# Performance work log

Measured on AMD Instinct MI355X. Metric: run time of the kernel, lower is better.

Reference implementation:

```python
import jax, jax.numpy as jnp
import numpy as np

G = 8          # grid_size
N = G * G      # 64 nodes
DEG = 17       # neighbors per node for 8x8 sudoku (2x4 boxes)
STEPS = 32
H = 96         # hidden_dim
E = 16         # embed_size
B = 16         # batch


def sudoku_edges():
    # row (7) + col (7) + 2x4 box (7) neighbors, set-union -> 17 per node
    idx = np.arange(N).reshape(G, G)
    nb = []
    for j in range(N):
        r, c = j // G, j % G
        br, bc = (r // 2) * 2, (c // 4) * 4
        s = set(idx[r, :].tolist()) | set(idx[:, c].tolist()) | set(idx[br:br + 2, bc:bc + 4].flatten().tolist())
        s.discard(j)
        nb.append(sorted(s))
    return np.asarray(nb, dtype=np.int32)  # [64, 17]


def setup_inputs() -> dict:
    key = jax.random.key(0)
    ks = jax.random.split(key, 16)
    sc = 0.05
    inp = {
        "x": jax.random.randint(ks[0], (B, G, G), 0, G + 1),            # given digits, 0 = blank
        "target": jax.random.randint(ks[1], (B, G, G), 0, G) + 1,       # solutions in 1..8
        "edges": jnp.asarray(sudoku_edges()),                            # [64, 17] int32
        "digit_emb": jax.random.normal(ks[2], (G + 1, E), jnp.float32) * sc,
        "row_emb": jax.random.normal(ks[3], (G, E), jnp.float32) * sc,
        "col_emb": jax.random.normal(ks[4], (G, E), jnp.float32) * sc,
        "in0_W": jax.random.normal(ks[5], (3 * E, H), jnp.float32) * sc,
        "in0_b": jnp.zeros((H,), jnp.float32),
        "in_Ws": jax.random.normal(ks[6], (3, H, H), jnp.float32) * sc,
        "in_bs": jnp.zeros((3, H), jnp.float32),
        "msg0_W": jax.random.normal(ks[7], (2 * H, H), jnp.float32) * sc,
        "msg0_b": jnp.zeros((H,), jnp.float32),
        "msg_Ws": jax.random.normal(ks[8], (3, H, H), jnp.float32) * sc,
        "msg_bs": jnp.zeros((3, H), jnp.float32),
        "W_ih": jax.random.normal(ks[9], (2 * H, 4 * H), jnp.float32) * sc,
        "W_hh": jax.random.normal(ks[10], (H, 4 * H), jnp.float32) * sc,
        "b_ih": jnp.zeros((4 * H,), jnp.float32),
        "b_hh": jnp.zeros((4 * H,), jnp.float32),
        "pred_W": jax.random.normal(ks[11], (H, G), jnp.float32) * sc,
        "pred_b": jnp.zeros((G,), jnp.float32),
    }
    return inp


def _mlp(z, W0, b0, Ws, bs):
    # Linear -> ReLU -> Linear -> ReLU -> Linear -> ReLU -> Linear (def_MLP)
    z = jax.nn.relu(z @ W0 + b0)
    z = jax.nn.relu(z @ Ws[0] + bs[0])
    z = jax.nn.relu(z @ Ws[1] + bs[1])
    return z @ Ws[2] + bs[2]


def reference(x, target, edges, digit_emb, row_emb, col_emb,
              in0_W, in0_b, in_Ws, in_bs,
              msg0_W, msg0_b, msg_Ws, msg_bs,
              W_ih, W_hh, b_ih, b_hh, pred_W, pred_b):
    bsz = x.shape[0]
    xf = x.reshape(bsz, N)
    tgt = target.reshape(bsz, N) - 1                      # labels 0..7

    de = digit_emb[xf]                                    # [B,64,E]
    re = row_emb[jnp.repeat(jnp.arange(G), G)]            # [64,E]
    ce = col_emb[jnp.tile(jnp.arange(G), G)]              # [64,E]
    feat = jnp.concatenate([de,
                            jnp.broadcast_to(re[None], (bsz, N, E)),
                            jnp.broadcast_to(ce[None], (bsz, N, E))], axis=-1)
    xin = _mlp(feat, in0_W, in0_b, in_Ws, in_bs)          # [B,64,H]

    h0 = jnp.zeros((bsz, N, H), jnp.float32)
    s0 = jnp.zeros((bsz * N, H), jnp.float32)

    def step(carry, _):
        h, s, loss = carry
        # gather-by-edge message passing
        h_edges = h[:, edges]                                             # [B,64,17,H]
        h_self = jnp.broadcast_to(h[:, :, None, :], (bsz, N, DEG, H))
        msg = _mlp(jnp.concatenate([h_edges, h_self], -1),
                   msg0_W, msg0_b, msg_Ws, msg_bs).sum(axis=2)            # [B,64,H]
        # LSTMCell update
        lstm_in = jnp.concatenate([msg, xin], -1).reshape(bsz * N, 2 * H)
        gates = lstm_in @ W_ih + b_ih + h.reshape(bsz * N, H) @ W_hh + b_hh
        i, f, g, o = jnp.split(gates, 4, axis=-1)
        s2 = jax.nn.sigmoid(f) * s + jax.nn.sigmoid(i) * jnp.tanh(g)
        h2 = (jax.nn.sigmoid(o) * jnp.tanh(s2)).reshape(bsz, N, H)
        # per-step prediction / loss / accuracy
        logp = jax.nn.log_softmax(h2 @ pred_W + pred_b, axis=-1)          # [B,64,8]
        pred = jnp.argmax(logp, axis=-1)
        acc = jnp.mean(jnp.all(pred == tgt, axis=1).astype(jnp.float32))
        loss_n = -jnp.sum(jnp.take_along_axis(logp, tgt[..., None], -1)) / (bsz * N)
        return (h2, s2, loss + loss_n), acc

    (h, s, loss), accs = jax.lax.scan(step, (h0, s0, jnp.float32(0.0)), None, length=STEPS)
    loss = loss / STEPS
    final_pred = jnp.argmax(h @ pred_W + pred_b, axis=-1)                 # [B,64]
    return loss, accs, final_pred
```

## Files before the change

### kernel.cpp

```cpp
#include <hip/hip_runtime.h>

#define DEG 17
#define NSTEPS 32
#define HD 96
#define BB 16
#define NN 64
#define NODES (BB*NN)
#define Z1STR 80
#define Z2STR 84

#define WS_H      0
#define WS_S      98304
#define WS_U0     196608
#define WS_U1     393216
#define WS_XIN    590352
#define WS_GX     688656
#define WS_W1P    1081872
#define WS_W2P    1094160
#define WS_LOSSP  1106448
#define WS_CNTP   1114640

__global__ void wpad_kernel(const float* __restrict__ msg_Ws,
                            float* __restrict__ W1p, float* __restrict__ W2p)
{
  const int k = blockIdx.x;
  const int tid = threadIdx.x;
  const int jg = tid >> 3, jj = tid & 7;
  float v1 = 0.f, v2 = 0.f;
  if (jj < 6) {
    v1 = msg_Ws[k*96 + jg*6 + jj];
    v2 = msg_Ws[9216 + k*96 + jg*6 + jj];
  }
  W1p[k*128 + tid] = v1;
  W2p[k*128 + tid] = v2;
}

__global__ void init_kernel(
    const int* __restrict__ x,
    const float* __restrict__ digit_emb,
    const float* __restrict__ row_emb,
    const float* __restrict__ col_emb,
    const float* __restrict__ in0_W,
    const float* __restrict__ in0_b,
    const float* __restrict__ in_Ws,
    const float* __restrict__ in_bs,
    float* __restrict__ xin)
{
  const int node = blockIdx.x;
  const int j = threadIdx.x;
  const int n = node & 63;
  const int r = n >> 3, c = n & 7;
  __shared__ float feat[48];
  __shared__ float za[HD];
  __shared__ float zb[HD];
  if (j < 16)      feat[j] = digit_emb[x[node]*16 + j];
  else if (j < 32) feat[j] = row_emb[r*16 + (j-16)];
  else if (j < 48) feat[j] = col_emb[c*16 + (j-32)];
  __syncthreads();
  float a = in0_b[j];
  for (int k = 0; k < 48; ++k) a = fmaf(feat[k], in0_W[k*HD + j], a);
  za[j] = fmaxf(a, 0.f);
  __syncthreads();
  a = in_bs[j];
  for (int k = 0; k < HD; ++k) a = fmaf(za[k], in_Ws[k*HD + j], a);
  zb[j] = fmaxf(a, 0.f);
  __syncthreads();
  a = in_bs[HD + j];
  for (int k = 0; k < HD; ++k) a = fmaf(zb[k], in_Ws[9216 + k*HD + j], a);
  za[j] = fmaxf(a, 0.f);
  __syncthreads();
  a = in_bs[2*HD + j];
  for (int k = 0; k < HD; ++k) a = fmaf(za[k], in_Ws[2*9216 + k*HD + j], a);
  xin[node*HD + j] = a;
}

__global__ __launch_bounds__(384) void gx_kernel(
    const float* __restrict__ xin, const float* __restrict__ W_ih,
    const float* __restrict__ b_ih, const float* __restrict__ b_hh,
    float* __restrict__ gx)
{
  __shared__ float xs[4*HD];
  const int tid = threadIdx.x;
  const int base = blockIdx.x * 4;
  {
    const int m = tid / HD, k = tid - m*HD;
    xs[m*HD + k] = xin[(base+m)*HD + k];
  }
  __syncthreads();
  const int j = tid;
  float a0 = b_ih[j] + b_hh[j], a1 = a0, a2 = a0, a3 = a0;
  for (int k = 0; k < HD; ++k) {
    const float w = W_ih[(96+k)*384 + j];
    a0 = fmaf(xs[k], w, a0);
    a1 = fmaf(xs[HD+k], w, a1);
    a2 = fmaf(xs[2*HD+k], w, a2);
    a3 = fmaf(xs[3*HD+k], w, a3);
  }
  gx[(base+0)*384 + j] = a0;
  gx[(base+1)*384 + j] = a1;
  gx[(base+2)*384 + j] = a2;
  gx[(base+3)*384 + j] = a3;
}

__global__ __launch_bounds__(384) void step_kernel(
    const float* __restrict__ u_prev, float* __restrict__ u_next,
    float* __restrict__ h, float* __restrict__ s,
    const float* __restrict__ gx,
    const int* __restrict__ edges,
    const float* __restrict__ W1p, const float* __restrict__ W2p,
    const float* __restrict__ msg0_W, const float* __restrict__ msg0_b,
    const float* __restrict__ msg_Ws, const float* __restrict__ msg_bs,
    const float* __restrict__ W_ih, const float* __restrict__ W_hh,
    const float* __restrict__ pred_W, const float* __restrict__ pred_b,
    const int* __restrict__ target,
    float* __restrict__ lossP, int* __restrict__ cntP,
    float* __restrict__ final_pred_out, int step)
{
  __shared__ float sm[15744];
  float* const z1s = sm;
  float* const z2s = sm + 7680;
  float* const s3t   = sm;
  float* const msgh  = sm + 384;
  float* const h2t   = sm + 1152;
  float* const lgt   = sm + 1536;
  float* const gates = sm + 1568;
  float* const P3    = sm + 3104;
  float* const PL = z2s;
  float* const PU = z2s;

  const int tid = threadIdx.x;
  const int blk = blockIdx.x;
  const int base = blk * 4;
  const int bb = blk >> 4;
  const int nbase = (blk & 15) * 4;

  {
    const int m = tid / HD, k = tid - m*HD;
    const float usv = u_prev[(base+m)*192 + 96 + k];
    const float b0v = msg0_b[k];
    z1s[k*Z1STR + m*20 + 17] = 0.f;
    z1s[k*Z1STR + m*20 + 18] = 0.f;
    z1s[k*Z1STR + m*20 + 19] = 0.f;
    const int erow = (nbase + m) * DEG;
    #pragma unroll 1
    for (int r = 0; r < DEG; ++r) {
      const int nbr = edges[erow + r];
      const float ue = u_prev[(bb*64 + nbr)*192 + k];
      z1s[k*Z1STR + m*20 + r] = fmaxf(ue + usv + b0v, 0.f);
    }
  }
  __syncthreads();

  if (tid < 320) {
    const int jg = tid & 15, dg = tid >> 4;
    const int j6 = jg*6, j8 = jg*8, dg4 = dg*4;
    float acc[4][6];
    #pragma unroll
    for (int dd = 0; dd < 4; ++dd)
      #pragma unroll
      for (int jj = 0; jj < 6; ++jj) acc[dd][jj] = 0.f;
    #pragma unroll 4
    for (int k = 0; k < HD; ++k) {
      const float4 z = *(const float4*)&z1s[k*Z1STR + dg4];
      const float* wp = W1p + k*128 + j8;
      const float4 wa = *(const float4*)wp;
      const float2 wb = *(const float2*)(wp + 4);
      const float ze[4] = {z.x, z.y, z.z, z.w};
      const float we[6] = {wa.x, wa.y, wa.z, wa.w, wb.x, wb.y};
      #pragma unroll
      for (int dd = 0; dd < 4; ++dd)
        #pragma unroll
        for (int jj = 0; jj < 6; ++jj)
          acc[dd][jj] = fmaf(ze[dd], we[jj], acc[dd][jj]);
    }
    #pragma unroll
    for (int jj = 0; jj < 6; ++jj) {
      const float b1 = msg_bs[j6 + jj];
      float4 q;
      q.x = fmaxf(acc[0][jj] + b1, 0.f);
      q.y = fmaxf(acc[1][jj] + b1, 0.f);
      q.z = fmaxf(acc[2][jj] + b1, 0.f);
      q.w = fmaxf(acc[3][jj] + b1, 0.f);
      *(float4*)&z2s[(j6+jj)*Z2STR + dg4] = q;
    }
  }
  __syncthreads();

  {
    s3t[tid] = 0.f;
    const int m = tid / HD, k = tid - m*HD;
    msgh[(96+k)*4 + m] = h[(base+m)*HD + k];
  }
  __syncthreads();

  if (tid < 320) {
    const int jg = tid & 15, dg = tid >> 4;
    const int j6 = jg*6, j8 = jg*8, dg4 = dg*4;
    const int nd = dg / 5, dgl = dg - nd*5;
    float acc[4][6];
    #pragma unroll
    for (int dd = 0; dd < 4; ++dd)
      #pragma unroll
      for (int jj = 0; jj < 6; ++jj) acc[dd][jj] = 0.f;
    #pragma unroll 4
    for (int k = 0; k < HD; ++k) {
      const float4 z = *(const float4*)&z2s[k*Z2STR + dg4];
      const float* wp = W2p + k*128 + j8;
      const float4 wa = *(const float4*)wp;
      const float2 wb = *(const float2*)(wp + 4);
      const float ze[4] = {z.x, z.y, z.z, z.w};
      const float we[6] = {wa.x, wa.y, wa.z, wa.w, wb.x, wb.y};
      #pragma unroll
      for (int dd = 0; dd < 4; ++dd)
        #pragma unroll
        for (int jj = 0; jj < 6; ++jj)
          acc[dd][jj] = fmaf(ze[dd], we[jj], acc[dd][jj]);
    }
    const int nvalid = (dgl < 4) ? 4 : 1;
    #pragma unroll
    for (int jj = 0; jj < 6; ++jj) {
      const float b2 = msg_bs[96 + j6 + jj];
      float p = 0.f;
      #pragma unroll
      for (int dd = 0; dd < 4; ++dd)
        if (dd < nvalid) p += fmaxf(acc[dd][jj] + b2, 0.f);
      atomicAdd(&s3t[(j6+jj)*4 + nd], p);
    }
  }
  __syncthreads();

  if (tid < 192) {
    const int jg = tid % 24, kq = tid / 24;
    const int j4 = jg*4, k0 = kq*12;
    const float* W3 = msg_Ws + 2*9216;
    float acc[4][4];
    #pragma unroll
    for (int m = 0; m < 4; ++m)
      #pragma unroll
      for (int jj = 0; jj < 4; ++jj) acc[m][jj] = 0.f;
    #pragma unroll 4
    for (int kk = 0; kk < 12; ++kk) {
      const int k = k0 + kk;
      const float4 sv = *(const float4*)&s3t[k*4];
      const float4 wv = *(const float4*)&W3[k*96 + j4];
      const float se[4] = {sv.x, sv.y, sv.z, sv.w};
      const float we[4] = {wv.x, wv.y, wv.z, wv.w};
      #pragma unroll
      for (int m = 0; m < 4; ++m)
        #pragma unroll
        for (int jj = 0; jj < 4; ++jj)
          acc[m][jj] = fmaf(se[m], we[jj], acc[m][jj]);
    }
    #pragma unroll
    for (int m = 0; m < 4; ++m) {
      float4 q = {acc[m][0], acc[m][1], acc[m][2], acc[m][3]};
      *(float4*)&P3[(kq*4 + m)*96 + j4] = q;
    }
  }
  __syncthreads();
  {
    const int m = tid / HD, j = tid - m*HD;
    float v = 17.f * msg_bs[192 + j];
    #pragma unroll
    for (int kq = 0; kq < 8; ++kq) v += P3[(kq*4 + m)*96 + j];
    msgh[j*4 + m] = v;
  }
  __syncthreads();

  if (tid < 192) {
    const int jg = tid % 48, kq = tid / 48;
    const int j8 = jg*8, k0 = kq*48;
    const float* Wb = (kq < 2) ? (W_ih + j8) : (W_hh + j8 - 96*384);
    float acc[4][8];
    #pragma unroll
    for (int m = 0; m < 4; ++m)
      #pragma unroll
      for (int jj = 0; jj < 8; ++jj) acc[m][jj] = 0.f;
    #pragma unroll 2
    for (int k = k0; k < k0 + 48; ++k) {
      const float4 iv = *(const float4*)&msgh[k*4];
      const float* wp = Wb + k*384;
      const float4 wa = *(const float4*)wp;
      const float4 wc = *(const float4*)(wp + 4);
      const float ie[4] = {iv.x, iv.y, iv.z, iv.w};
      const float we[8] = {wa.x, wa.y, wa.z, wa.w, wc.x, wc.y, wc.z, wc.w};
      #pragma unroll
      for (int m = 0; m < 4; ++m)
        #pragma unroll
        for (int jj = 0; jj < 8; ++jj)
          acc[m][jj] = fmaf(ie[m], we[jj], acc[m][jj]);
    }
    #pragma unroll
    for (int m = 0; m < 4; ++m) {
      float4 qa = {acc[m][0], acc[m][1], acc[m][2], acc[m][3]};
      float4 qb = {acc[m][4], acc[m][5], acc[m][6], acc[m][7]};
      *(float4*)&PL[(kq*4 + m)*384 + j8] = qa;
      *(float4*)&PL[(kq*4 + m)*384 + j8 + 4] = qb;
    }
  }
  __syncthreads();
  {
    const int j = tid;
    #pragma unroll
    for (int m = 0; m < 4; ++m) {
      float g = gx[(base+m)*384 + j];
      #pragma unroll
      for (int kq = 0; kq < 4; ++kq) g += PL[(kq*4 + m)*384 + j];
      gates[m*384 + j] = g;
    }
  }
  __syncthreads();

  {
    const int m = tid / HD, hj = tid - m*HD;
    const int node = base + m;
    const float gi = gates[m*384 + hj];
    const float gf = gates[m*384 + 96 + hj];
    const float gg = gates[m*384 + 192 + hj];
    const float go = gates[m*384 + 288 + hj];
    const float sv = s[node*HD + hj];
    const float ig = 1.f/(1.f + expf(-gi));
    const float fg = 1.f/(1.f + expf(-gf));
    const float cg = tanhf(gg);
    const float og = 1.f/(1.f + expf(-go));
    const float s2 = fg*sv + ig*cg;
    const float h2 = og*tanhf(s2);
    s[node*HD + hj] = s2;
    h[node*HD + hj] = h2;
    h2t[hj*4 + m] = h2;
  }
  __syncthreads();

  if (tid < 192) {
    const int jg = tid % 24, kq = tid / 24;
    const int j8 = jg*8, k0 = kq*12;
    const float* Wb = (j8 < 96) ? (msg0_W + j8) : (msg0_W + 9216 + j8 - 96);
    float acc[4][8];
    #pragma unroll
    for (int m = 0; m < 4; ++m)
      #pragma unroll
      for (int jj = 0; jj < 8; ++jj) acc[m][jj] = 0.f;
    #pragma unroll 4
    for (int kk = 0; kk < 12; ++kk) {
      const int k = k0 + kk;
      const float4 iv = *(const float4*)&h2t[k*4];
      const float* wp = Wb + k*96;
      const float4 wa = *(const float4*)wp;
      const float4 wc = *(const float4*)(wp + 4);
      const float ie[4] = {iv.x, iv.y, iv.z, iv.w};
      const float we[8] = {wa.x, wa.y, wa.z, wa.w, wc.x, wc.y, wc.z, wc.w};
      #pragma unroll
      for (int m = 0; m < 4; ++m)
        #pragma unroll
        for (int jj = 0; jj < 8; ++jj)
          acc[m][jj] = fmaf(ie[m], we[jj], acc[m][jj]);
    }
    #pragma unroll
    for (int m = 0; m < 4; ++m) {
      float4 qa = {acc[m][0], acc[m][1], acc[m][2], acc[m][3]};
      float4 qb = {acc[m][4], acc[m][5], acc[m][6], acc[m][7]};
      *(float4*)&PU[(kq*4 + m)*192 + j8] = qa;
      *(float4*)&PU[(kq*4 + m)*192 + j8 + 4] = qb;
    }
  }
  __syncthreads();
  {
    const int j = tid % 192, mh = tid / 192;
    #pragma unroll
    for (int t = 0; t < 2; ++t) {
      const int mm = mh + 2*t;
      float v = 0.f;
      #pragma unroll
      for (int kq = 0; kq < 8; ++kq) v += PU[(kq*4 + mm)*192 + j];
      u_next[(base+mm)*192 + j] = v;
    }
  }

  if (tid < 256) {
    const int m = tid >> 6, c = (tid >> 3) & 7, kq = tid & 7;
    float p = 0.f;
    #pragma unroll
    for (int kk = 0; kk < 12; ++kk) {
      const int k = kq*12 + kk;
      p = fmaf(h2t[k*4 + m], pred_W[k*8 + c], p);
    }
    p += __shfl_xor(p, 1);
    p += __shfl_xor(p, 2);
    p += __shfl_xor(p, 4);
    if (kq == 0) lgt[m*8 + c] = p + pred_b[c];
  }
  __syncthreads();
  if (tid < 4) {
    const int m = tid;
    const int node = base + m;
    float mx = lgt[m*8];
    int pred = 0;
    #pragma unroll
    for (int c = 1; c < 8; ++c) {
      const float v = lgt[m*8 + c];
      if (v > mx) { mx = v; pred = c; }
    }
    float sum = 0.f;
    #pragma unroll
    for (int c = 0; c < 8; ++c) sum += expf(lgt[m*8 + c] - mx);
    const float lse = mx + logf(sum);
    const int tgt = target[node] - 1;
    lgt[16 + m] = lse - lgt[m*8 + tgt];
    lgt[20 + m] = (pred == tgt) ? 1.f : 0.f;
    if (step == NSTEPS-1) final_pred_out[node] = (float)pred;
    if (m == 0) {
      lossP[step*256 + blk] = lgt[16] + lgt[17] + lgt[18] + lgt[19];
      cntP[step*256 + blk] = (int)(lgt[20] + lgt[21] + lgt[22] + lgt[23]);
    }
  }
}

__global__ void finalize_kernel(const float* __restrict__ lossP,
                                const int* __restrict__ cntP,
                                float* __restrict__ out)
{
  __shared__ float sl[32];
  const int tid = threadIdx.x;
  const int st = tid >> 3, q = tid & 7;
  float lsum = 0.f;
  for (int i = 0; i < 32; ++i) lsum += lossP[st*256 + q*32 + i];
  lsum += __shfl_xor(lsum, 1);
  lsum += __shfl_xor(lsum, 2);
  lsum += __shfl_xor(lsum, 4);
  if (q == 0) sl[st] = lsum;
  float okc = 0.f;
  #pragma unroll
  for (int t = 0; t < 2; ++t) {
    const int bbat = q + 8*t;
    int c = 0;
    for (int i = 0; i < 16; ++i) c += cntP[st*256 + bbat*16 + i];
    okc += (c == 64) ? 1.f : 0.f;
  }
  okc += __shfl_xor(okc, 1);
  okc += __shfl_xor(okc, 2);
  okc += __shfl_xor(okc, 4);
  if (q == 0) out[1 + st] = okc / 16.f;
  __syncthreads();
  if (tid == 0) {
    float tot = 0.f;
    for (int i = 0; i < 32; ++i) tot += sl[i];
    out[0] = tot / ((float)NODES * (float)NSTEPS);
  }
}

extern "C" void kernel_launch(void* const* d_in, const int* in_sizes, int n_in,
                              void* d_out, int out_size, void* d_ws, size_t ws_size,
                              hipStream_t stream) {
  const int*   x         = (const int*)  d_in[0];
  const int*   target    = (const int*)  d_in[1];
  const int*   edges     = (const int*)  d_in[2];
  const float* digit_emb = (const float*)d_in[3];
  const float* row_emb   = (const float*)d_in[4];
  const float* col_emb   = (const float*)d_in[5];
  const float* in0_W     = (const float*)d_in[6];
  const float* in0_b     = (const float*)d_in[7];
  const float* in_Ws     = (const float*)d_in[8];
  const float* in_bs     = (const float*)d_in[9];
  const float* msg0_W    = (const float*)d_in[10];
  const float* msg0_b    = (const float*)d_in[11];
  const float* msg_Ws    = (const float*)d_in[12];
  const float* msg_bs    = (const float*)d_in[13];
  const float* W_ih      = (const float*)d_in[14];
  const float* W_hh      = (const float*)d_in[15];
  const float* pred_W    = (const float*)d_in[18];
  const float* pred_b    = (const float*)d_in[19];

  float* ws    = (float*)d_ws;
  float* hbuf  = ws + WS_H;
  float* sbuf  = ws + WS_S;
  float* u0    = ws + WS_U0;
  float* u1    = ws + WS_U1;
  float* xin   = ws + WS_XIN;
  float* gxb   = ws + WS_GX;
  float* W1p   = ws + WS_W1P;
  float* W2p   = ws + WS_W2P;
  float* lossP = ws + WS_LOSSP;
  int*   cntP  = (int*)(ws + WS_CNTP);

  hipMemsetAsync(d_ws, 0, (size_t)393216*sizeof(float), stream);

  wpad_kernel<<<96, 128, 0, stream>>>(msg_Ws, W1p, W2p);
  init_kernel<<<NODES, HD, 0, stream>>>(x, digit_emb, row_emb, col_emb,
                                        in0_W, in0_b, in_Ws, in_bs, xin);
  gx_kernel<<<256, 384, 0, stream>>>(xin, W_ih,
                                     (const float*)d_in[16], (const float*)d_in[17],
                                     gxb);

  float* outp = (float*)d_out;
  for (int st = 0; st < NSTEPS; ++st) {
    const float* up = (st & 1) ? u1 : u0;
    float*       un = (st & 1) ? u0 : u1;
    step_kernel<<<256, 384, 0, stream>>>(
        up, un, hbuf, sbuf, gxb, edges,
        W1p, W2p, msg0_W, msg0_b, msg_Ws, msg_bs,
        W_ih, W_hh, pred_W, pred_b,
        target, lossP, cntP, outp + 1 + NSTEPS, st);
  }

  finalize_kernel<<<1, 256, 0, stream>>>(lossP, cntP, outp);
}
```

Measured before the change: 1.170 ms.

## Fuse all recurrent steps into one persistent kernel with per-batch grid barriers

New measurement: 1.097 ms. 6.2% less time.

```diff
diff --git a/kernel.cpp b/kernel.cpp
--- a/kernel.cpp
+++ b/kernel.cpp
@@ -3,37 +3,34 @@
 #define DEG 17
 #define NSTEPS 32
 #define HD 96
-#define BB 16
-#define NN 64
-#define NODES (BB*NN)
-#define Z1STR 80
-#define Z2STR 84
-
-#define WS_H      0
-#define WS_S      98304
-#define WS_U0     196608
-#define WS_U1     393216
-#define WS_XIN    590352
-#define WS_GX     688656
-#define WS_W1P    1081872
-#define WS_W2P    1094160
-#define WS_LOSSP  1106448
-#define WS_CNTP   1114640
-
-__global__ void wpad_kernel(const float* __restrict__ msg_Ws,
-                            float* __restrict__ W1p, float* __restrict__ W2p)
-{
-  const int k = blockIdx.x;
-  const int tid = threadIdx.x;
-  const int jg = tid >> 3, jj = tid & 7;
-  float v1 = 0.f, v2 = 0.f;
-  if (jj < 6) {
-    v1 = msg_Ws[k*96 + jg*6 + jj];
-    v2 = msg_Ws[9216 + k*96 + jg*6 + jj];
-  }
-  W1p[k*128 + tid] = v1;
-  W2p[k*128 + tid] = v2;
-}
+#define NODES 1024
+
+#define WS_U0     0
+#define WS_BAR    196608
+#define WS_U1     196864
+#define WS_XIN    393472
+#define WS_GX     491776
+#define WS_LOSSP  884992
+#define WS_CNTP   893184
+
+#define Z1    0
+#define Z2    7680
+#define P3    0
+#define PL    0
+#define PU    0
+#define W1L   15360
+#define W2L   24576
+#define GXL   33792
+#define GATES 35328
+#define MSGH  36864
+#define S3T   37632
+#define H2T   38016
+#define SLC   38400
+#define MSGB  38784
+#define M0B   39072
+#define LGT   39168
+#define NBRI  39200
+#define SMTOT 39280
 
 __global__ void init_kernel(
     const int* __restrict__ x,
@@ -44,7 +41,9 @@
     const float* __restrict__ in0_b,
     const float* __restrict__ in_Ws,
     const float* __restrict__ in_bs,
-    float* __restrict__ xin)
+    const float* __restrict__ msg0_b,
+    float* __restrict__ xin,
+    float* __restrict__ u0)
 {
   const int node = blockIdx.x;
   const int j = threadIdx.x;
@@ -56,6 +55,7 @@
   if (j < 16)      feat[j] = digit_emb[x[node]*16 + j];
   else if (j < 32) feat[j] = row_emb[r*16 + (j-16)];
   else if (j < 48) feat[j] = col_emb[c*16 + (j-32)];
+  u0[node*192 + 96 + j] = msg0_b[j];
   __syncthreads();
   float a = in0_b[j];
   for (int k = 0; k < 48; ++k) a = fmaf(feat[k], in0_W[k*HD + j], a);
@@ -102,315 +102,333 @@
   gx[(base+3)*384 + j] = a3;
 }
 
-__global__ __launch_bounds__(384) void step_kernel(
-    const float* __restrict__ u_prev, float* __restrict__ u_next,
-    float* __restrict__ h, float* __restrict__ s,
-    const float* __restrict__ gx,
+__global__ __launch_bounds__(512, 1) void solve_kernel(
     const int* __restrict__ edges,
-    const float* __restrict__ W1p, const float* __restrict__ W2p,
     const float* __restrict__ msg0_W, const float* __restrict__ msg0_b,
     const float* __restrict__ msg_Ws, const float* __restrict__ msg_bs,
     const float* __restrict__ W_ih, const float* __restrict__ W_hh,
     const float* __restrict__ pred_W, const float* __restrict__ pred_b,
     const int* __restrict__ target,
+    const float* __restrict__ gx,
+    float* __restrict__ u0, float* __restrict__ u1,
+    int* bar,
     float* __restrict__ lossP, int* __restrict__ cntP,
-    float* __restrict__ final_pred_out, int step)
+    float* __restrict__ final_pred_out)
 {
-  __shared__ float sm[15744];
-  float* const z1s = sm;
-  float* const z2s = sm + 7680;
-  float* const s3t   = sm;
-  float* const msgh  = sm + 384;
-  float* const h2t   = sm + 1152;
-  float* const lgt   = sm + 1536;
-  float* const gates = sm + 1568;
-  float* const P3    = sm + 3104;
-  float* const PL = z2s;
-  float* const PU = z2s;
+  __shared__ float sm[SMTOT];
 
   const int tid = threadIdx.x;
   const int blk = blockIdx.x;
-  const int base = blk * 4;
-  const int bb = blk >> 4;
-  const int nbase = (blk & 15) * 4;
-
-  {
-    const int m = tid / HD, k = tid - m*HD;
-    const float usv = u_prev[(base+m)*192 + 96 + k];
-    const float b0v = msg0_b[k];
-    z1s[k*Z1STR + m*20 + 17] = 0.f;
-    z1s[k*Z1STR + m*20 + 18] = 0.f;
-    z1s[k*Z1STR + m*20 + 19] = 0.f;
-    const int erow = (nbase + m) * DEG;
-    #pragma unroll 1
-    for (int r = 0; r < DEG; ++r) {
-      const int nbr = edges[erow + r];
-      const float ue = u_prev[(bb*64 + nbr)*192 + k];
-      z1s[k*Z1STR + m*20 + r] = fmaxf(ue + usv + b0v, 0.f);
-    }
-  }
-  __syncthreads();
-
-  if (tid < 320) {
-    const int jg = tid & 15, dg = tid >> 4;
-    const int j6 = jg*6, j8 = jg*8, dg4 = dg*4;
-    float acc[4][6];
-    #pragma unroll
-    for (int dd = 0; dd < 4; ++dd)
-      #pragma unroll
-      for (int jj = 0; jj < 6; ++jj) acc[dd][jj] = 0.f;
-    #pragma unroll 4
-    for (int k = 0; k < HD; ++k) {
-      const float4 z = *(const float4*)&z1s[k*Z1STR + dg4];
-      const float* wp = W1p + k*128 + j8;
-      const float4 wa = *(const float4*)wp;
-      const float2 wb = *(const float2*)(wp + 4);
-      const float ze[4] = {z.x, z.y, z.z, z.w};
-      const float we[6] = {wa.x, wa.y, wa.z, wa.w, wb.x, wb.y};
-      #pragma unroll
-      for (int dd = 0; dd < 4; ++dd)
-        #pragma unroll
-        for (int jj = 0; jj < 6; ++jj)
-          acc[dd][jj] = fmaf(ze[dd], we[jj], acc[dd][jj]);
-    }
-    #pragma unroll
-    for (int jj = 0; jj < 6; ++jj) {
-      const float b1 = msg_bs[j6 + jj];
-      float4 q;
-      q.x = fmaxf(acc[0][jj] + b1, 0.f);
-      q.y = fmaxf(acc[1][jj] + b1, 0.f);
-      q.z = fmaxf(acc[2][jj] + b1, 0.f);
-      q.w = fmaxf(acc[3][jj] + b1, 0.f);
-      *(float4*)&z2s[(j6+jj)*Z2STR + dg4] = q;
-    }
-  }
-  __syncthreads();
-
-  {
-    s3t[tid] = 0.f;
-    const int m = tid / HD, k = tid - m*HD;
-    msgh[(96+k)*4 + m] = h[(base+m)*HD + k];
-  }
-  __syncthreads();
-
-  if (tid < 320) {
-    const int jg = tid & 15, dg = tid >> 4;
-    const int j6 = jg*6, j8 = jg*8, dg4 = dg*4;
-    const int nd = dg / 5, dgl = dg - nd*5;
-    float acc[4][6];
-    #pragma unroll
-    for (int dd = 0; dd < 4; ++dd)
-      #pragma unroll
-      for (int jj = 0; jj < 6; ++jj) acc[dd][jj] = 0.f;
-    #pragma unroll 4
-    for (int k = 0; k < HD; ++k) {
-      const float4 z = *(const float4*)&z2s[k*Z2STR + dg4];
-      const float* wp = W2p + k*128 + j8;
-      const float4 wa = *(const float4*)wp;
-      const float2 wb = *(const float2*)(wp + 4);
-      const float ze[4] = {z.x, z.y, z.z, z.w};
-      const float we[6] = {wa.x, wa.y, wa.z, wa.w, wb.x, wb.y};
-      #pragma unroll
-      for (int dd = 0; dd < 4; ++dd)
-        #pragma unroll
-        for (int jj = 0; jj < 6; ++jj)
-          acc[dd][jj] = fmaf(ze[dd], we[jj], acc[dd][jj]);
-    }
-    const int nvalid = (dgl < 4) ? 4 : 1;
-    #pragma unroll
-    for (int jj = 0; jj < 6; ++jj) {
-      const float b2 = msg_bs[96 + j6 + jj];
-      float p = 0.f;
-      #pragma unroll
-      for (int dd = 0; dd < 4; ++dd)
-        if (dd < nvalid) p += fmaxf(acc[dd][jj] + b2, 0.f);
-      atomicAdd(&s3t[(j6+jj)*4 + nd], p);
-    }
-  }
-  __syncthreads();
-
-  if (tid < 192) {
-    const int jg = tid % 24, kq = tid / 24;
-    const int j4 = jg*4, k0 = kq*12;
-    const float* W3 = msg_Ws + 2*9216;
-    float acc[4][4];
-    #pragma unroll
-    for (int m = 0; m < 4; ++m)
-      #pragma unroll
-      for (int jj = 0; jj < 4; ++jj) acc[m][jj] = 0.f;
-    #pragma unroll 4
-    for (int kk = 0; kk < 12; ++kk) {
-      const int k = k0 + kk;
-      const float4 sv = *(const float4*)&s3t[k*4];
-      const float4 wv = *(const float4*)&W3[k*96 + j4];
-      const float se[4] = {sv.x, sv.y, sv.z, sv.w};
-      const float we[4] = {wv.x, wv.y, wv.z, wv.w};
-      #pragma unroll
-      for (int m = 0; m < 4; ++m)
-        #pragma unroll
-        for (int jj = 0; jj < 4; ++jj)
-          acc[m][jj] = fmaf(se[m], we[jj], acc[m][jj]);
-    }
-    #pragma unroll
-    for (int m = 0; m < 4; ++m) {
-      float4 q = {acc[m][0], acc[m][1], acc[m][2], acc[m][3]};
-      *(float4*)&P3[(kq*4 + m)*96 + j4] = q;
-    }
-  }
-  __syncthreads();
-  {
-    const int m = tid / HD, j = tid - m*HD;
-    float v = 17.f * msg_bs[192 + j];
-    #pragma unroll
-    for (int kq = 0; kq < 8; ++kq) v += P3[(kq*4 + m)*96 + j];
-    msgh[j*4 + m] = v;
-  }
-  __syncthreads();
-
-  if (tid < 192) {
-    const int jg = tid % 48, kq = tid / 48;
-    const int j8 = jg*8, k0 = kq*48;
-    const float* Wb = (kq < 2) ? (W_ih + j8) : (W_hh + j8 - 96*384);
-    float acc[4][8];
-    #pragma unroll
-    for (int m = 0; m < 4; ++m)
-      #pragma unroll
-      for (int jj = 0; jj < 8; ++jj) acc[m][jj] = 0.f;
-    #pragma unroll 2
-    for (int k = k0; k < k0 + 48; ++k) {
-      const float4 iv = *(const float4*)&msgh[k*4];
-      const float* wp = Wb + k*384;
-      const float4 wa = *(const float4*)wp;
-      const float4 wc = *(const float4*)(wp + 4);
-      const float ie[4] = {iv.x, iv.y, iv.z, iv.w};
-      const float we[8] = {wa.x, wa.y, wa.z, wa.w, wc.x, wc.y, wc.z, wc.w};
-      #pragma unroll
-      for (int m = 0; m < 4; ++m)
-        #pragma unroll
-        for (int jj = 0; jj < 8; ++jj)
-          acc[m][jj] = fmaf(ie[m], we[jj], acc[m][jj]);
-    }
-    #pragma unroll
-    for (int m = 0; m < 4; ++m) {
-      float4 qa = {acc[m][0], acc[m][1], acc[m][2], acc[m][3]};
-      float4 qb = {acc[m][4], acc[m][5], acc[m][6], acc[m][7]};
-      *(float4*)&PL[(kq*4 + m)*384 + j8] = qa;
-      *(float4*)&PL[(kq*4 + m)*384 + j8 + 4] = qb;
-    }
-  }
-  __syncthreads();
-  {
-    const int j = tid;
-    #pragma unroll
-    for (int m = 0; m < 4; ++m) {
-      float g = gx[(base+m)*384 + j];
-      #pragma unroll
-      for (int kq = 0; kq < 4; ++kq) g += PL[(kq*4 + m)*384 + j];
-      gates[m*384 + j] = g;
-    }
-  }
-  __syncthreads();
-
-  {
-    const int m = tid / HD, hj = tid - m*HD;
-    const int node = base + m;
-    const float gi = gates[m*384 + hj];
-    const float gf = gates[m*384 + 96 + hj];
-    const float gg = gates[m*384 + 192 + hj];
-    const float go = gates[m*384 + 288 + hj];
-    const float sv = s[node*HD + hj];
-    const float ig = 1.f/(1.f + expf(-gi));
-    const float fg = 1.f/(1.f + expf(-gf));
-    const float cg = tanhf(gg);
-    const float og = 1.f/(1.f + expf(-go));
-    const float s2 = fg*sv + ig*cg;
-    const float h2 = og*tanhf(s2);
-    s[node*HD + hj] = s2;
-    h[node*HD + hj] = h2;
-    h2t[hj*4 + m] = h2;
-  }
-  __syncthreads();
-
-  if (tid < 192) {
-    const int jg = tid % 24, kq = tid / 24;
-    const int j8 = jg*8, k0 = kq*12;
-    const float* Wb = (j8 < 96) ? (msg0_W + j8) : (msg0_W + 9216 + j8 - 96);
-    float acc[4][8];
-    #pragma unroll
-    for (int m = 0; m < 4; ++m)
-      #pragma unroll
-      for (int jj = 0; jj < 8; ++jj) acc[m][jj] = 0.f;
-    #pragma unroll 4
-    for (int kk = 0; kk < 12; ++kk) {
-      const int k = k0 + kk;
-      const float4 iv = *(const float4*)&h2t[k*4];
-      const float* wp = Wb + k*96;
-      const float4 wa = *(const float4*)wp;
-      const float4 wc = *(const float4*)(wp + 4);
-      const float ie[4] = {iv.x, iv.y, iv.z, iv.w};
-      const float we[8] = {wa.x, wa.y, wa.z, wa.w, wc.x, wc.y, wc.z, wc.w};
-      #pragma unroll
-      for (int m = 0; m < 4; ++m)
-        #pragma unroll
-        for (int jj = 0; jj < 8; ++jj)
-          acc[m][jj] = fmaf(ie[m], we[jj], acc[m][jj]);
-    }
-    #pragma unroll
-    for (int m = 0; m < 4; ++m) {
-      float4 qa = {acc[m][0], acc[m][1], acc[m][2], acc[m][3]};
-      float4 qb = {acc[m][4], acc[m][5], acc[m][6], acc[m][7]};
-      *(float4*)&PU[(kq*4 + m)*192 + j8] = qa;
-      *(float4*)&PU[(kq*4 + m)*192 + j8 + 4] = qb;
-    }
-  }
-  __syncthreads();
-  {
-    const int j = tid % 192, mh = tid / 192;
-    #pragma unroll
-    for (int t = 0; t < 2; ++t) {
-      const int mm = mh + 2*t;
-      float v = 0.f;
-      #pragma unroll
-      for (int kq = 0; kq < 8; ++kq) v += PU[(kq*4 + mm)*192 + j];
-      u_next[(base+mm)*192 + j] = v;
-    }
-  }
-
-  if (tid < 256) {
-    const int m = tid >> 6, c = (tid >> 3) & 7, kq = tid & 7;
-    float p = 0.f;
-    #pragma unroll
-    for (int kk = 0; kk < 12; ++kk) {
-      const int k = kq*12 + kk;
-      p = fmaf(h2t[k*4 + m], pred_W[k*8 + c], p);
-    }
-    p += __shfl_xor(p, 1);
-    p += __shfl_xor(p, 2);
-    p += __shfl_xor(p, 4);
-    if (kq == 0) lgt[m*8 + c] = p + pred_b[c];
-  }
-  __syncthreads();
-  if (tid < 4) {
-    const int m = tid;
-    const int node = base + m;
-    float mx = lgt[m*8];
-    int pred = 0;
-    #pragma unroll
-    for (int c = 1; c < 8; ++c) {
-      const float v = lgt[m*8 + c];
-      if (v > mx) { mx = v; pred = c; }
-    }
-    float sum = 0.f;
-    #pragma unroll
-    for (int c = 0; c < 8; ++c) sum += expf(lgt[m*8 + c] - mx);
-    const float lse = mx + logf(sum);
-    const int tgt = target[node] - 1;
-    lgt[16 + m] = lse - lgt[m*8 + tgt];
-    lgt[20 + m] = (pred == tgt) ? 1.f : 0.f;
-    if (step == NSTEPS-1) final_pred_out[node] = (float)pred;
-    if (m == 0) {
-      lossP[step*256 + blk] = lgt[16] + lgt[17] + lgt[18] + lgt[19];
-      cntP[step*256 + blk] = (int)(lgt[20] + lgt[21] + lgt[22] + lgt[23]);
+  const int bb = blk & 15;
+  const int grp = blk >> 4;
+  const int nbase = grp * 4;
+  const int base = bb*64 + nbase;
+
+  for (int i = tid*4; i < 9216; i += 2048) {
+    *(float4*)&sm[W1L + i] = *(const float4*)&msg_Ws[i];
+    *(float4*)&sm[W2L + i] = *(const float4*)&msg_Ws[9216 + i];
+  }
+  #pragma unroll
+  for (int t = 0; t < 3; ++t) {
+    const int idx = t*512 + tid;
+    sm[GXL + idx] = gx[base*384 + idx];
+  }
+  if (tid < 288) sm[MSGB + tid] = msg_bs[tid];
+  if (tid < 96)  sm[M0B + tid]  = msg0_b[tid];
+  if (tid < 80) {
+    const int m = tid / 20, r = tid % 20;
+    ((int*)&sm[NBRI])[tid] = (r < DEG) ? (bb*64 + edges[(nbase+m)*DEG + r])*192 : -1;
+  }
+  if (tid < 384) {
+    sm[SLC + tid] = 0.f;
+    sm[MSGH + 384 + tid] = 0.f;
+  }
+  __syncthreads();
+
+  const float* uP = u0;
+  float*       uN = u1;
+
+  for (int st = 0; st < NSTEPS; ++st) {
+    if (tid < 480) {
+      const int row = tid % 80;
+      const int kh  = tid / 80;
+      const int m = row / 20;
+      const int k0 = kh * 16;
+      const int nb = ((const int*)&sm[NBRI])[row];
+      if (nb >= 0) {
+        const float* ue = uP + nb + k0;
+        const float* us = uP + (base+m)*192 + 96 + k0;
+        #pragma unroll
+        for (int t = 0; t < 4; ++t) {
+          const float4 a = *(const float4*)(ue + 4*t);
+          const float4 b = *(const float4*)(us + 4*t);
+          sm[Z1 + (k0+4*t+0)*80 + row] = fmaxf(a.x + b.x, 0.f);
+          sm[Z1 + (k0+4*t+1)*80 + row] = fmaxf(a.y + b.y, 0.f);
+          sm[Z1 + (k0+4*t+2)*80 + row] = fmaxf(a.z + b.z, 0.f);
+          sm[Z1 + (k0+4*t+3)*80 + row] = fmaxf(a.w + b.w, 0.f);
+        }
+      } else {
+        #pragma unroll
+        for (int t = 0; t < 16; ++t) sm[Z1 + (k0+t)*80 + row] = 0.f;
+      }
+    } else {
+      const int i = tid - 480;
+      #pragma unroll
+      for (int t = 0; t < 12; ++t) sm[S3T + t*32 + i] = 0.f;
+    }
+    __syncthreads();
+
+    if (tid < 480) {
+      const int jg = tid % 24, dg = tid / 24;
+      const int j4 = jg*4, d4 = dg*4;
+      float acc[4][4] = {{0.f}};
+      #pragma unroll 4
+      for (int k = 0; k < 96; ++k) {
+        const float4 z = *(const float4*)&sm[Z1 + k*80 + d4];
+        const float4 w = *(const float4*)&sm[W1L + k*96 + j4];
+        const float ze[4] = {z.x, z.y, z.z, z.w};
+        const float we[4] = {w.x, w.y, w.z, w.w};
+        #pragma unroll
+        for (int dd = 0; dd < 4; ++dd)
+          #pragma unroll
+          for (int jj = 0; jj < 4; ++jj)
+            acc[dd][jj] = fmaf(ze[dd], we[jj], acc[dd][jj]);
+      }
+      #pragma unroll
+      for (int jj = 0; jj < 4; ++jj) {
+        const float b1 = sm[MSGB + j4 + jj];
+        float4 q;
+        q.x = fmaxf(acc[0][jj] + b1, 0.f);
+        q.y = fmaxf(acc[1][jj] + b1, 0.f);
+        q.z = fmaxf(acc[2][jj] + b1, 0.f);
+        q.w = fmaxf(acc[3][jj] + b1, 0.f);
+        *(float4*)&sm[Z2 + (j4+jj)*80 + d4] = q;
+      }
+    }
+    __syncthreads();
+
+    if (tid < 480) {
+      const int jg = tid % 24, dg = tid / 24;
+      const int j4 = jg*4, d4 = dg*4;
+      float acc[4][4] = {{0.f}};
+      #pragma unroll 4
+      for (int k = 0; k < 96; ++k) {
+        const float4 z = *(const float4*)&sm[Z2 + k*80 + d4];
+        const float4 w = *(const float4*)&sm[W2L + k*96 + j4];
+        const float ze[4] = {z.x, z.y, z.z, z.w};
+        const float we[4] = {w.x, w.y, w.z, w.w};
+        #pragma unroll
+        for (int dd = 0; dd < 4; ++dd)
+          #pragma unroll
+          for (int jj = 0; jj < 4; ++jj)
+            acc[dd][jj] = fmaf(ze[dd], we[jj], acc[dd][jj]);
+      }
+      const int nd = d4 / 20;
+      const int r0 = d4 - nd*20;
+      #pragma unroll
+      for (int jj = 0; jj < 4; ++jj) {
+        const float b2 = sm[MSGB + 96 + j4 + jj];
+        float p = 0.f;
+        #pragma unroll
+        for (int dd = 0; dd < 4; ++dd)
+          if (r0 + dd < DEG) p += fmaxf(acc[dd][jj] + b2, 0.f);
+        atomicAdd(&sm[S3T + (j4+jj)*4 + nd], p);
+      }
+    }
+    __syncthreads();
+
+    if (tid < 384) {
+      const int jg = tid % 24, kq = tid / 24;
+      const int j4 = jg*4, k0 = kq*6;
+      const float* W3 = msg_Ws + 2*9216;
+      float acc[4][4] = {{0.f}};
+      #pragma unroll
+      for (int kk = 0; kk < 6; ++kk) {
+        const int k = k0 + kk;
+        const float4 sv = *(const float4*)&sm[S3T + k*4];
+        const float4 wv = *(const float4*)&W3[k*96 + j4];
+        const float se[4] = {sv.x, sv.y, sv.z, sv.w};
+        const float we[4] = {wv.x, wv.y, wv.z, wv.w};
+        #pragma unroll
+        for (int m = 0; m < 4; ++m)
+          #pragma unroll
+          for (int jj = 0; jj < 4; ++jj)
+            acc[m][jj] = fmaf(se[m], we[jj], acc[m][jj]);
+      }
+      #pragma unroll
+      for (int m = 0; m < 4; ++m) {
+        float4 q = {acc[m][0], acc[m][1], acc[m][2], acc[m][3]};
+        *(float4*)&sm[P3 + (kq*4 + m)*96 + j4] = q;
+      }
+    }
+    __syncthreads();
+    if (tid < 384) {
+      const int m = tid / 96, j = tid % 96;
+      float v = 17.f * sm[MSGB + 192 + j];
+      #pragma unroll
+      for (int kq = 0; kq < 16; ++kq) v += sm[P3 + (kq*4 + m)*96 + j];
+      sm[MSGH + j*4 + m] = v;
+    }
+    __syncthreads();
+
+    {
+      const int jg = tid & 63, kq = tid >> 6;
+      const int j6 = jg*6, k0 = kq*24;
+      const float* Wb = (k0 < 96) ? (W_ih + (size_t)k0*384) : (W_hh + (size_t)(k0-96)*384);
+      float acc[4][6] = {{0.f}};
+      #pragma unroll 4
+      for (int kk = 0; kk < 24; ++kk) {
+        const float4 iv = *(const float4*)&sm[MSGH + (k0+kk)*4];
+        const float* wp = Wb + kk*384 + j6;
+        const float2 wa = *(const float2*)wp;
+        const float2 wb2 = *(const float2*)(wp + 2);
+        const float2 wc = *(const float2*)(wp + 4);
+        const float ie[4] = {iv.x, iv.y, iv.z, iv.w};
+        const float we[6] = {wa.x, wa.y, wb2.x, wb2.y, wc.x, wc.y};
+        #pragma unroll
+        for (int m = 0; m < 4; ++m)
+          #pragma unroll
+          for (int jj = 0; jj < 6; ++jj)
+            acc[m][jj] = fmaf(ie[m], we[jj], acc[m][jj]);
+      }
+      #pragma unroll
+      for (int m = 0; m < 4; ++m) {
+        float2 qa = {acc[m][0], acc[m][1]};
+        float2 qb = {acc[m][2], acc[m][3]};
+        float2 qc = {acc[m][4], acc[m][5]};
+        *(float2*)&sm[PL + (kq*4 + m)*384 + j6]     = qa;
+        *(float2*)&sm[PL + (kq*4 + m)*384 + j6 + 2] = qb;
+        *(float2*)&sm[PL + (kq*4 + m)*384 + j6 + 4] = qc;
+      }
+    }
+    __syncthreads();
+    {
+      #pragma unroll
+      for (int t = 0; t < 3; ++t) {
+        const int idx = t*512 + tid;
+        const int m = idx / 384, j = idx - m*384;
+        float gv = sm[GXL + idx];
+        #pragma unroll
+        for (int kq = 0; kq < 8; ++kq) gv += sm[PL + (kq*4 + m)*384 + j];
+        sm[GATES + idx] = gv;
+      }
+    }
+    __syncthreads();
+
+    if (tid < 384) {
+      const int m = tid / 96, hj = tid - m*96;
+      const float gi = sm[GATES + m*384 + hj];
+      const float gf = sm[GATES + m*384 + 96 + hj];
+      const float gg = sm[GATES + m*384 + 192 + hj];
+      const float go = sm[GATES + m*384 + 288 + hj];
+      const float sv = sm[SLC + tid];
+      const float ig = 1.f/(1.f + expf(-gi));
+      const float fg = 1.f/(1.f + expf(-gf));
+      const float cg = tanhf(gg);
+      const float og = 1.f/(1.f + expf(-go));
+      const float s2 = fg*sv + ig*cg;
+      const float h2 = og*tanhf(s2);
+      sm[SLC + tid] = s2;
+      sm[H2T + hj*4 + m] = h2;
+      sm[MSGH + (96+hj)*4 + m] = h2;
+    }
+    __syncthreads();
+
+    {
+      const int jg = tid & 31, kq = tid >> 5;
+      const int j6 = jg*6, k0 = kq*6;
+      const float* Wb = (j6 < 96) ? (msg0_W + j6) : (msg0_W + 9216 + j6 - 96);
+      float acc[4][6] = {{0.f}};
+      #pragma unroll
+      for (int kk = 0; kk < 6; ++kk) {
+        const int k = k0 + kk;
+        const float4 iv = *(const float4*)&sm[H2T + k*4];
+        const float* wp = Wb + k*96;
+        const float2 wa = *(const float2*)wp;
+        const float2 wb2 = *(const float2*)(wp + 2);
+        const float2 wc = *(const float2*)(wp + 4);
+        const float ie[4] = {iv.x, iv.y, iv.z, iv.w};
+        const float we[6] = {wa.x, wa.y, wb2.x, wb2.y, wc.x, wc.y};
+        #pragma unroll
+        for (int m = 0; m < 4; ++m)
+          #pragma unroll
+          for (int jj = 0; jj < 6; ++jj)
+            acc[m][jj] = fmaf(ie[m], we[jj], acc[m][jj]);
+      }
+      #pragma unroll
+      for (int m = 0; m < 4; ++m) {
+        float2 qa = {acc[m][0], acc[m][1]};
+        float2 qb = {acc[m][2], acc[m][3]};
+        float2 qc = {acc[m][4], acc[m][5]};
+        *(float2*)&sm[PU + (kq*4 + m)*192 + j6]     = qa;
+        *(float2*)&sm[PU + (kq*4 + m)*192 + j6 + 2] = qb;
+        *(float2*)&sm[PU + (kq*4 + m)*192 + j6 + 4] = qc;
+      }
+    }
+    __syncthreads();
+    {
+      #pragma unroll
+      for (int t = 0; t < 2; ++t) {
+        const int idx = t*512 + tid;
+        if (idx < 768) {
+          const int m = idx / 192, j = idx - m*192;
+          float v = (j >= 96) ? sm[M0B + j - 96] : 0.f;
+          #pragma unroll
+          for (int kq = 0; kq < 16; ++kq) v += sm[PU + (kq*4 + m)*192 + j];
+          uN[(base+m)*192 + j] = v;
+        }
+      }
+      if (tid >= 384) {
+        const int t2 = tid - 384;
+        const int m = t2 >> 5, c = (t2 >> 2) & 7, kq2 = t2 & 3;
+        float p = 0.f;
+        #pragma unroll
+        for (int kk = 0; kk < 24; ++kk) {
+          const int k = kq2*24 + kk;
+          p = fmaf(sm[H2T + k*4 + m], pred_W[k*8 + c], p);
+        }
+        p += __shfl_xor(p, 1);
+        p += __shfl_xor(p, 2);
+        if (kq2 == 0) sm[LGT + m*8 + c] = p + pred_b[c];
+      }
+    }
+    __syncthreads();
+
+    if (tid < 4) {
+      const int m = tid;
+      const int node = base + m;
+      float mx = sm[LGT + m*8];
+      int pred = 0;
+      #pragma unroll
+      for (int c = 1; c < 8; ++c) {
+        const float v = sm[LGT + m*8 + c];
+        if (v > mx) { mx = v; pred = c; }
+      }
+      float sum = 0.f;
+      #pragma unroll
+      for (int c = 0; c < 8; ++c) sum += expf(sm[LGT + m*8 + c] - mx);
+      const float lse = mx + logf(sum);
+      const int tgt = target[node] - 1;
+      sm[LGT + 16 + m] = lse - sm[LGT + m*8 + tgt];
+      sm[LGT + 20 + m] = (pred == tgt) ? 1.f : 0.f;
+      if (st == NSTEPS-1) final_pred_out[node] = (float)pred;
+      if (m == 0) {
+        lossP[st*256 + blk] = sm[LGT+16] + sm[LGT+17] + sm[LGT+18] + sm[LGT+19];
+        cntP[st*256 + blk] = (int)(sm[LGT+20] + sm[LGT+21] + sm[LGT+22] + sm[LGT+23]);
+      }
+    }
+
+    if (st < NSTEPS-1) {
+      __syncthreads();
+      if (tid == 0) {
+        __hip_atomic_fetch_add(&bar[bb*16], 1, __ATOMIC_RELEASE, __HIP_MEMORY_SCOPE_AGENT);
+        const int want = 16*(st+1);
+        while (__hip_atomic_load(&bar[bb*16], __ATOMIC_RELAXED, __HIP_MEMORY_SCOPE_AGENT) < want)
+          __builtin_amdgcn_s_sleep(2);
+        __threadfence();
+      }
+      __syncthreads();
+      float* tp = (float*)uP; uP = uN; uN = tp;
     }
   }
 }
@@ -433,7 +451,7 @@
   for (int t = 0; t < 2; ++t) {
     const int bbat = q + 8*t;
     int c = 0;
-    for (int i = 0; i < 16; ++i) c += cntP[st*256 + bbat*16 + i];
+    for (int i = 0; i < 16; ++i) c += cntP[st*256 + i*16 + bbat];
     okc += (c == 64) ? 1.f : 0.f;
   }
   okc += __shfl_xor(okc, 1);
@@ -467,40 +485,32 @@
   const float* msg_bs    = (const float*)d_in[13];
   const float* W_ih      = (const float*)d_in[14];
   const float* W_hh      = (const float*)d_in[15];
+  const float* b_ih      = (const float*)d_in[16];
+  const float* b_hh      = (const float*)d_in[17];
   const float* pred_W    = (const float*)d_in[18];
   const float* pred_b    = (const float*)d_in[19];
 
   float* ws    = (float*)d_ws;
-  float* hbuf  = ws + WS_H;
-  float* sbuf  = ws + WS_S;
   float* u0    = ws + WS_U0;
+  int*   bar   = (int*)(ws + WS_BAR);
   float* u1    = ws + WS_U1;
   float* xin   = ws + WS_XIN;
   float* gxb   = ws + WS_GX;
-  float* W1p   = ws + WS_W1P;
-  float* W2p   = ws + WS_W2P;
   float* lossP = ws + WS_LOSSP;
   int*   cntP  = (int*)(ws + WS_CNTP);
 
-  hipMemsetAsync(d_ws, 0, (size_t)393216*sizeof(float), stream);
-
-  wpad_kernel<<<96, 128, 0, stream>>>(msg_Ws, W1p, W2p);
+  hipMemsetAsync(d_ws, 0, (size_t)(196608 + 256)*sizeof(float), stream);
+
   init_kernel<<<NODES, HD, 0, stream>>>(x, digit_emb, row_emb, col_emb,
-                                        in0_W, in0_b, in_Ws, in_bs, xin);
-  gx_kernel<<<256, 384, 0, stream>>>(xin, W_ih,
-                                     (const float*)d_in[16], (const float*)d_in[17],
-                                     gxb);
+                                        in0_W, in0_b, in_Ws, in_bs,
+                                        msg0_b, xin, u0);
+  gx_kernel<<<256, 384, 0, stream>>>(xin, W_ih, b_ih, b_hh, gxb);
 
   float* outp = (float*)d_out;
-  for (int st = 0; st < NSTEPS; ++st) {
-    const float* up = (st & 1) ? u1 : u0;
-    float*       un = (st & 1) ? u0 : u1;
-    step_kernel<<<256, 384, 0, stream>>>(
-        up, un, hbuf, sbuf, gxb, edges,
-        W1p, W2p, msg0_W, msg0_b, msg_Ws, msg_bs,
-        W_ih, W_hh, pred_W, pred_b,
-        target, lossP, cntP, outp + 1 + NSTEPS, st);
-  }
+  solve_kernel<<<256, 512, 0, stream>>>(
+      edges, msg0_W, msg0_b, msg_Ws, msg_bs,
+      W_ih, W_hh, pred_W, pred_b, target, gxb,
+      u0, u1, bar, lossP, cntP, outp + 1 + NSTEPS);
 
   finalize_kernel<<<1, 256, 0, stream>>>(lossP, cntP, outp);
 }
```
